# Performance work log

Hardware: AMD Instinct MI355X
Metric: run time of the kernel (lower is better)

The kernel has to match this reference:

```python
import jax, jax.numpy as jnp
import numpy as np
from jax import lax

ALPHABET = 64
E = 1024   # embedding_dim == output_dim == HIDDEN
H = 1024
MSG_LEN = 20
BOS = ALPHABET          # 64
PAD = ALPHABET + 1      # 65
EOS = 0
B = 4096


def setup_inputs() -> dict:
    key = jax.random.key(0)
    ks = jax.random.split(key, 12)
    def u(k, shape, s):
        return jax.random.uniform(k, shape, jnp.float32, -s, s)
    sE = 1.0 / np.sqrt(E)
    sH = 1.0 / np.sqrt(H)
    embed = jax.random.normal(ks[0], (ALPHABET + 2, E), jnp.float32)
    embed = embed.at[PAD].set(0.0)  # padding_idx row is zero
    return dict(
        encoded=jax.random.normal(ks[1], (B, E), jnp.float32),
        embed=embed,
        W_ih=u(ks[2], (4 * H, E), sH), W_hh=u(ks[3], (4 * H, H), sH),
        b_ih=u(ks[4], (4 * H,), sH), b_hh=u(ks[5], (4 * H,), sH),
        W_cell=u(ks[6], (E, E), sE), b_cell=u(ks[7], (E,), sE),
        W_hid=u(ks[8], (E, E), sE), b_hid=u(ks[9], (E,), sE),
        W_act=u(ks[10], (ALPHABET, E), sE), b_act=u(ks[11], (ALPHABET,), sE),
    )


def reference(encoded, embed, W_ih, W_hh, b_ih, b_hh,
              W_cell, b_cell, W_hid, b_hid, W_act, b_act):
    b = encoded.shape[0]
    # torch passes state=(cell, hidden) to nn.LSTM, which reads (h0, c0):
    h0 = encoded @ W_cell.T + b_cell
    c0 = encoded @ W_hid.T + b_hid
    last0 = jnp.full((b,), BOS, jnp.int32)
    stopped0 = jnp.zeros((b,), bool)
    keys = jax.random.split(jax.random.key(42), MSG_LEN)
    bias = b_ih + b_hh

    def step(carry, k):
        h, c, last, stopped = carry
        # embedding lookup; zero the pad row (padding_idx semantics)
        x = embed[last] * (last != PAD)[:, None].astype(embed.dtype)
        gates = x @ W_ih.T + h @ W_hh.T + bias          # [b, 4H], gate order i,f,g,o
        i, f, g, o = jnp.split(gates, 4, axis=-1)
        c2 = jax.nn.sigmoid(f) * c + jax.nn.sigmoid(i) * jnp.tanh(g)
        h2 = jax.nn.sigmoid(o) * jnp.tanh(c2)
        logits = h2 @ W_act.T + b_act                   # [b, ALPHABET]
        action = jax.random.categorical(k, logits)      # training-mode sample
        logp = jax.nn.log_softmax(logits)
        live = (~stopped).astype(logits.dtype)
        ent = -jnp.sum(jnp.exp(logp) * logp, axis=-1) * live
        lp = jnp.take_along_axis(logp, action[:, None], axis=1)[:, 0] * live
        action = jnp.where(stopped, PAD, action).astype(jnp.int32)
        stopped2 = stopped | (action == EOS)
        return (h2, c2, action, stopped2), (action, lp, ent)

    _, (msg, lps, ents) = lax.scan(step, (h0, c0, last0, stopped0), keys)
    msg = msg.T          # [b, MSG_LEN]
    log_probs = lps.T    # [b, MSG_LEN]
    ents = ents.T        # [b, MSG_LEN]
    message_len = jnp.sum(msg != PAD, axis=1, keepdims=True)  # count of non-pad symbols
    entropy = jnp.sum(ents, axis=1, keepdims=True) / message_len.astype(ents.dtype)
    return entropy, log_probs, msg, message_len
```

## Files before the change

### kernel.cpp

```cpp
#include <hip/hip_runtime.h>
#include <stdint.h>

#define ALPHA 64
#define EDIM 1024
#define G4 4096
#define BATCH 4096
#define TLEN 20
#define BOS_TOK 64
#define PAD_TOK 65
#define EOS_TOK 0

__device__ __forceinline__ void threefry2x32(uint32_t k0, uint32_t k1,
                                             uint32_t& x0, uint32_t& x1) {
  uint32_t ks[3] = {k0, k1, k0 ^ k1 ^ 0x1BD11BDAu};
  const int rot0[4] = {13, 15, 26, 6};
  const int rot1[4] = {17, 29, 16, 24};
  x0 += ks[0];
  x1 += ks[1];
#pragma unroll
  for (int i = 0; i < 5; ++i) {
    const int* rr = (i & 1) ? rot1 : rot0;
#pragma unroll
    for (int j = 0; j < 4; ++j) {
      x0 += x1;
      x1 = (x1 << rr[j]) | (x1 >> (32 - rr[j]));
      x1 ^= x0;
    }
    x0 += ks[(i + 1) % 3];
    x1 += ks[(i + 2) % 3] + (uint32_t)(i + 1);
  }
}

__global__ void init_kernel(uint32_t* __restrict__ keyA, uint32_t* __restrict__ keyB,
                            int* __restrict__ last, int* __restrict__ stopped,
                            double* __restrict__ ent_sum, int* __restrict__ len_sum) {
  int i = blockIdx.x * 256 + threadIdx.x;
  if (i < BATCH) {
    last[i] = BOS_TOK;
    stopped[i] = 0;
    ent_sum[i] = 0.0;
    len_sum[i] = 0;
  }
  if (i < TLEN) {
    uint32_t x0 = 0u, x1 = (uint32_t)i;
    threefry2x32(0u, 42u, x0, x1);
    keyA[i] = x0;
    keyB[i] = x1;
  }
}

__global__ void transpose_wact(const float* __restrict__ W, float* __restrict__ Wt) {
  int i = blockIdx.x * 256 + threadIdx.x;
  if (i < ALPHA * EDIM) {
    int a = i >> 10, k = i & 1023;
    Wt[(size_t)k * ALPHA + a] = W[i];
  }
}

template <int MODE>
__global__ __launch_bounds__(256) void gemm_nt(
    const float* __restrict__ A, const float* __restrict__ Bw, float* __restrict__ C,
    int M, int N, int K,
    const float* __restrict__ bias1, const float* __restrict__ bias2,
    const float* __restrict__ eg, const int* __restrict__ lastIdx) {
  __shared__ float As[16][132];
  __shared__ float Bs[16][132];
  const int t = threadIdx.x;
  const int bm = blockIdx.y * 128;
  const int bn = blockIdx.x * 128;
  const int tx = t & 15, ty = t >> 4;

  float acc[8][8];
#pragma unroll
  for (int i = 0; i < 8; ++i)
#pragma unroll
    for (int j = 0; j < 8; ++j) acc[i][j] = 0.0f;

  const int sr = t >> 1;
  const int sc = (t & 1) << 3;
  const float* ap = A + (size_t)(bm + sr) * K + sc;
  const float* bp = Bw + (size_t)(bn + sr) * K + sc;
  const bool aok = (bm + sr) < M;

  for (int k0 = 0; k0 < K; k0 += 16) {
    float4 av0 = {0.f, 0.f, 0.f, 0.f}, av1 = {0.f, 0.f, 0.f, 0.f};
    if (aok) {
      av0 = *(const float4*)(ap + k0);
      av1 = *(const float4*)(ap + k0 + 4);
    }
    float4 bv0 = *(const float4*)(bp + k0);
    float4 bv1 = *(const float4*)(bp + k0 + 4);
    __syncthreads();
    As[sc + 0][sr] = av0.x; As[sc + 1][sr] = av0.y; As[sc + 2][sr] = av0.z; As[sc + 3][sr] = av0.w;
    As[sc + 4][sr] = av1.x; As[sc + 5][sr] = av1.y; As[sc + 6][sr] = av1.z; As[sc + 7][sr] = av1.w;
    Bs[sc + 0][sr] = bv0.x; Bs[sc + 1][sr] = bv0.y; Bs[sc + 2][sr] = bv0.z; Bs[sc + 3][sr] = bv0.w;
    Bs[sc + 4][sr] = bv1.x; Bs[sc + 5][sr] = bv1.y; Bs[sc + 6][sr] = bv1.z; Bs[sc + 7][sr] = bv1.w;
    __syncthreads();
#pragma unroll
    for (int k = 0; k < 16; ++k) {
      float4 a0 = *(const float4*)&As[k][ty * 4];
      float4 a1 = *(const float4*)&As[k][ty * 4 + 64];
      float4 b0 = *(const float4*)&Bs[k][tx * 4];
      float4 b1 = *(const float4*)&Bs[k][tx * 4 + 64];
      float ar[8] = {a0.x, a0.y, a0.z, a0.w, a1.x, a1.y, a1.z, a1.w};
      float br[8] = {b0.x, b0.y, b0.z, b0.w, b1.x, b1.y, b1.z, b1.w};
#pragma unroll
      for (int i = 0; i < 8; ++i)
#pragma unroll
        for (int j = 0; j < 8; ++j) acc[i][j] = fmaf(ar[i], br[j], acc[i][j]);
    }
  }

#pragma unroll
  for (int i = 0; i < 8; ++i) {
    int mG = bm + ty * 4 + (i & 3) + ((i >> 2) << 6);
    if (mG >= M) continue;
    const float* egrow = nullptr;
    if (MODE == 1) egrow = eg + (size_t)lastIdx[mG] * G4;
#pragma unroll
    for (int j = 0; j < 8; ++j) {
      int nG = bn + tx * 4 + (j & 3) + ((j >> 2) << 6);
      float v;
      if (MODE == 0) {
        v = acc[i][j];
        if (bias1) v = __fadd_rn(v, bias1[nG]);
      } else {
        float bsum = __fadd_rn(bias1[nG], bias2[nG]);
        v = __fadd_rn(__fadd_rn(egrow[nG], acc[i][j]), bsum);
      }
      C[(size_t)mG * N + nG] = v;
    }
  }
}

__global__ __launch_bounds__(256) void lstm_pointwise(const float* __restrict__ gates,
                                                      float* __restrict__ h,
                                                      float* __restrict__ c) {
  int idx = blockIdx.x * 256 + threadIdx.x;
  int b = idx >> 10, jj = idx & 1023;
  const float* grow = gates + ((size_t)b << 12);
  float gi = grow[jj];
  float gf = grow[jj + 1024];
  float gg = grow[jj + 2048];
  float go = grow[jj + 3072];
  float cc = c[idx];
  float si = 1.0f / (__fadd_rn(1.0f, expf(-gi)));
  float sf = 1.0f / (__fadd_rn(1.0f, expf(-gf)));
  float so = 1.0f / (__fadd_rn(1.0f, expf(-go)));
  float c2 = __fadd_rn(__fmul_rn(sf, cc), __fmul_rn(si, tanhf(gg)));
  float h2 = __fmul_rn(so, tanhf(c2));
  c[idx] = c2;
  h[idx] = h2;
}

__global__ __launch_bounds__(256) void logits_sample(
    const float* __restrict__ h, const float* __restrict__ Wt,
    const float* __restrict__ b_act,
    const uint32_t* __restrict__ keyA, const uint32_t* __restrict__ keyB, int tstep,
    int* __restrict__ last, int* __restrict__ stopped,
    double* __restrict__ ent_sum, int* __restrict__ len_sum,
    float* __restrict__ out_lp, float* __restrict__ out_msg) {
  __shared__ float Ws[64][64];
  __shared__ float Hs[8][64];
  const int tid = threadIdx.x;
  const int wave = tid >> 6;
  const int lane = tid & 63;
  const int rowBase = blockIdx.x * 8;

  float acc0 = 0.0f, acc1 = 0.0f;
  for (int kp = 0; kp < EDIM; kp += 64) {
    __syncthreads();
    {
      const float4* src = (const float4*)(Wt + (size_t)kp * ALPHA);
      float4* dst = (float4*)&Ws[0][0];
#pragma unroll
      for (int q = 0; q < 4; ++q) dst[tid + q * 256] = src[tid + q * 256];
    }
    if (tid < 128) {
      int rr = tid >> 4;
      int cc = (tid & 15) << 2;
      *(float4*)&Hs[rr][cc] = *(const float4*)(h + (size_t)(rowBase + rr) * EDIM + kp + cc);
    }
    __syncthreads();
#pragma unroll
    for (int kk = 0; kk < 64; ++kk) {
      float w = Ws[kk][lane];
      acc0 = fmaf(Hs[wave * 2 + 0][kk], w, acc0);
      acc1 = fmaf(Hs[wave * 2 + 1][kk], w, acc1);
    }
  }

  const float ba = b_act[lane];
  const uint32_t k0 = keyA[tstep], k1 = keyB[tstep];
  float logitv[2] = {__fadd_rn(acc0, ba), __fadd_rn(acc1, ba)};

#pragma unroll
  for (int rsel = 0; rsel < 2; ++rsel) {
    const int b = rowBase + wave * 2 + rsel;
    const float logit = logitv[rsel];

    uint32_t m = ((uint32_t)b << 6) | (uint32_t)lane;
    uint32_t x0 = 0u, x1 = m;
    threefry2x32(k0, k1, x0, x1);
    uint32_t bits = x0 ^ x1;

    float f = __fsub_rn(__uint_as_float((bits >> 9) | 0x3F800000u), 1.0f);
    const float TINY = 1.17549435e-38f;
    float u = fmaxf(TINY, __fadd_rn(f, TINY));
    float gmb = -logf(-logf(u));
    float z = __fadd_rn(logit, gmb);

    float bv = z;
    int bi = lane;
#pragma unroll
    for (int off = 32; off > 0; off >>= 1) {
      float ov = __shfl_xor(bv, off, 64);
      int oi = __shfl_xor(bi, off, 64);
      if (ov > bv || (ov == bv && oi < bi)) { bv = ov; bi = oi; }
    }

    float mx = logit;
#pragma unroll
    for (int off = 32; off > 0; off >>= 1) mx = fmaxf(mx, __shfl_xor(mx, off, 64));
    float sh = __fsub_rn(logit, mx);
    float e = expf(sh);
    float s = e;
#pragma unroll
    for (int off = 32; off > 0; off >>= 1) s = __fadd_rn(s, __shfl_xor(s, off, 64));
    float ls = logf(s);
    float logp = __fsub_rn(sh, ls);

    float term = __fmul_rn(expf(logp), logp);
    float ts = term;
#pragma unroll
    for (int off = 32; off > 0; off >>= 1) ts = __fadd_rn(ts, __shfl_xor(ts, off, 64));

    float lp_taken = __shfl(logp, bi, 64);

    int st = stopped[b];
    float live = st ? 0.0f : 1.0f;
    int act = st ? PAD_TOK : bi;
    int st2 = (st || act == EOS_TOK) ? 1 : 0;

    if (lane == 0) {
      out_msg[(size_t)b * TLEN + tstep] = (float)act;
      out_lp[(size_t)b * TLEN + tstep] = __fmul_rn(lp_taken, live);
      ent_sum[b] += (double)__fmul_rn(-ts, live);
      len_sum[b] += (act != PAD_TOK) ? 1 : 0;
      last[b] = act;
      stopped[b] = st2;
    }
  }
}

__global__ void finalize_kernel(const double* __restrict__ ent_sum,
                                const int* __restrict__ len_sum,
                                float* __restrict__ out_ent, float* __restrict__ out_len) {
  int b = blockIdx.x * 256 + threadIdx.x;
  if (b < BATCH) {
    out_ent[b] = (float)(ent_sum[b] / (double)len_sum[b]);
    out_len[b] = (float)len_sum[b];
  }
}

extern "C" void kernel_launch(void* const* d_in, const int* in_sizes, int n_in,
                              void* d_out, int out_size, void* d_ws, size_t ws_size,
                              hipStream_t stream) {
  const float* encoded = (const float*)d_in[0];
  const float* embed = (const float*)d_in[1];
  const float* W_ih = (const float*)d_in[2];
  const float* W_hh = (const float*)d_in[3];
  const float* b_ih = (const float*)d_in[4];
  const float* b_hh = (const float*)d_in[5];
  const float* W_cell = (const float*)d_in[6];
  const float* b_cell = (const float*)d_in[7];
  const float* W_hid = (const float*)d_in[8];
  const float* b_hid = (const float*)d_in[9];
  const float* W_act = (const float*)d_in[10];
  const float* b_act = (const float*)d_in[11];

  float* out = (float*)d_out;
  float* out_ent = out;
  float* out_lp = out + BATCH;
  float* out_msg = out + BATCH + BATCH * TLEN;
  float* out_len = out + BATCH + 2 * BATCH * TLEN;

  char* ws = (char*)d_ws;
  size_t off = 0;
  auto alloc = [&](size_t bytes) -> void* {
    void* p = ws + off;
    off = (off + bytes + 255) & ~(size_t)255;
    return p;
  };
  float* h = (float*)alloc(sizeof(float) * (size_t)BATCH * EDIM);
  float* c = (float*)alloc(sizeof(float) * (size_t)BATCH * EDIM);
  float* gates = (float*)alloc(sizeof(float) * (size_t)BATCH * G4);
  float* eg = (float*)alloc(sizeof(float) * 66 * G4);
  float* Wt = (float*)alloc(sizeof(float) * EDIM * ALPHA);
  uint32_t* keyA = (uint32_t*)alloc(sizeof(uint32_t) * TLEN);
  uint32_t* keyB = (uint32_t*)alloc(sizeof(uint32_t) * TLEN);
  int* last = (int*)alloc(sizeof(int) * BATCH);
  int* stopped = (int*)alloc(sizeof(int) * BATCH);
  double* ent_s = (double*)alloc(sizeof(double) * BATCH);
  int* len_s = (int*)alloc(sizeof(int) * BATCH);
  (void)ws_size; (void)in_sizes; (void)n_in; (void)out_size;

  init_kernel<<<16, 256, 0, stream>>>(keyA, keyB, last, stopped, ent_s, len_s);
  transpose_wact<<<(ALPHA * EDIM) / 256, 256, 0, stream>>>(W_act, Wt);

  gemm_nt<0><<<dim3(32, 1), 256, 0, stream>>>(embed, W_ih, eg, 66, G4, EDIM,
                                              nullptr, nullptr, nullptr, nullptr);
  gemm_nt<0><<<dim3(8, 32), 256, 0, stream>>>(encoded, W_cell, h, BATCH, EDIM, EDIM,
                                              b_cell, nullptr, nullptr, nullptr);
  gemm_nt<0><<<dim3(8, 32), 256, 0, stream>>>(encoded, W_hid, c, BATCH, EDIM, EDIM,
                                              b_hid, nullptr, nullptr, nullptr);

  for (int t = 0; t < TLEN; ++t) {
    gemm_nt<1><<<dim3(32, 32), 256, 0, stream>>>(h, W_hh, gates, BATCH, G4, EDIM,
                                                 b_ih, b_hh, eg, last);
    lstm_pointwise<<<(BATCH * EDIM) / 256, 256, 0, stream>>>(gates, h, c);
    logits_sample<<<BATCH / 8, 256, 0, stream>>>(h, Wt, b_act, keyA, keyB, t,
                                                 last, stopped, ent_s, len_s,
                                                 out_lp, out_msg);
  }
  finalize_kernel<<<16, 256, 0, stream>>>(ent_s, len_s, out_ent, out_len);
}
```

Before: 9.178 ms.

## Fuse LSTM pointwise into recurrent GEMM epilogue with gate-interleaved tiles

Each GEMM tile now loads the i/f/g/o rows for 32 hidden units, so every thread holds all four gates for its outputs and applies the LSTM cell update in the epilogue. This removes the 64MB gates buffer write and read-back and one kernel launch per step. Because the fused kernel reads h while writing the new h, h is double-buffered. The epilogue now has strided global accesses to c and h and does transcendental work per thread inside the GEMM kernel.

After: 9.638 ms. +5.0%, slower.

```diff
diff --git a/kernel.cpp b/kernel.cpp
--- a/kernel.cpp
+++ b/kernel.cpp
@@ -57,12 +57,9 @@
   }
 }
 
-template <int MODE>
-__global__ __launch_bounds__(256) void gemm_nt(
+__global__ __launch_bounds__(256) void gemm_nt0(
     const float* __restrict__ A, const float* __restrict__ Bw, float* __restrict__ C,
-    int M, int N, int K,
-    const float* __restrict__ bias1, const float* __restrict__ bias2,
-    const float* __restrict__ eg, const int* __restrict__ lastIdx) {
+    int M, int N, int K, const float* __restrict__ bias1) {
   __shared__ float As[16][132];
   __shared__ float Bs[16][132];
   const int t = threadIdx.x;
@@ -115,42 +112,97 @@
   for (int i = 0; i < 8; ++i) {
     int mG = bm + ty * 4 + (i & 3) + ((i >> 2) << 6);
     if (mG >= M) continue;
-    const float* egrow = nullptr;
-    if (MODE == 1) egrow = eg + (size_t)lastIdx[mG] * G4;
 #pragma unroll
     for (int j = 0; j < 8; ++j) {
       int nG = bn + tx * 4 + (j & 3) + ((j >> 2) << 6);
-      float v;
-      if (MODE == 0) {
-        v = acc[i][j];
-        if (bias1) v = __fadd_rn(v, bias1[nG]);
-      } else {
-        float bsum = __fadd_rn(bias1[nG], bias2[nG]);
-        v = __fadd_rn(__fadd_rn(egrow[nG], acc[i][j]), bsum);
+      float v = acc[i][j];
+      if (bias1) v = __fadd_rn(v, bias1[nG]);
+      C[(size_t)mG * N + nG] = v;
+    }
+  }
+}
+
+__global__ __launch_bounds__(256) void gemm_lstm_fused(
+    const float* __restrict__ A, const float* __restrict__ Bw,
+    const float* __restrict__ eg, const int* __restrict__ lastIdx,
+    const float* __restrict__ b_ih, const float* __restrict__ b_hh,
+    float* __restrict__ hN, float* __restrict__ cst) {
+  __shared__ float As[16][132];
+  __shared__ float Bs[16][132];
+  const int t = threadIdx.x;
+  const int bm = blockIdx.y * 128;
+  const int j0 = blockIdx.x * 32;
+  const int tx = t & 15, ty = t >> 4;
+
+  float acc[8][8];
+#pragma unroll
+  for (int i = 0; i < 8; ++i)
+#pragma unroll
+    for (int j = 0; j < 8; ++j) acc[i][j] = 0.0f;
+
+  const int sr = t >> 1;
+  const int sc = (t & 1) << 3;
+  const float* ap = A + (size_t)(bm + sr) * EDIM + sc;
+  const float* bp = Bw + (size_t)((sr & 3) * EDIM + j0 + (sr >> 2)) * EDIM + sc;
+
+  float4 av0 = *(const float4*)(ap);
+  float4 av1 = *(const float4*)(ap + 4);
+  float4 bv0 = *(const float4*)(bp);
+  float4 bv1 = *(const float4*)(bp + 4);
+
+  for (int k0 = 0; k0 < EDIM; k0 += 16) {
+    __syncthreads();
+    As[sc + 0][sr] = av0.x; As[sc + 1][sr] = av0.y; As[sc + 2][sr] = av0.z; As[sc + 3][sr] = av0.w;
+    As[sc + 4][sr] = av1.x; As[sc + 5][sr] = av1.y; As[sc + 6][sr] = av1.z; As[sc + 7][sr] = av1.w;
+    Bs[sc + 0][sr] = bv0.x; Bs[sc + 1][sr] = bv0.y; Bs[sc + 2][sr] = bv0.z; Bs[sc + 3][sr] = bv0.w;
+    Bs[sc + 4][sr] = bv1.x; Bs[sc + 5][sr] = bv1.y; Bs[sc + 6][sr] = bv1.z; Bs[sc + 7][sr] = bv1.w;
+    if (k0 + 16 < EDIM) {
+      av0 = *(const float4*)(ap + k0 + 16);
+      av1 = *(const float4*)(ap + k0 + 20);
+      bv0 = *(const float4*)(bp + k0 + 16);
+      bv1 = *(const float4*)(bp + k0 + 20);
+    }
+    __syncthreads();
+#pragma unroll
+    for (int k = 0; k < 16; ++k) {
+      float4 a0 = *(const float4*)&As[k][ty * 4];
+      float4 a1 = *(const float4*)&As[k][ty * 4 + 64];
+      float4 b0 = *(const float4*)&Bs[k][tx * 4];
+      float4 b1 = *(const float4*)&Bs[k][tx * 4 + 64];
+      float ar[8] = {a0.x, a0.y, a0.z, a0.w, a1.x, a1.y, a1.z, a1.w};
+      float br[8] = {b0.x, b0.y, b0.z, b0.w, b1.x, b1.y, b1.z, b1.w};
+#pragma unroll
+      for (int i = 0; i < 8; ++i)
+#pragma unroll
+        for (int j = 0; j < 8; ++j) acc[i][j] = fmaf(ar[i], br[j], acc[i][j]);
+    }
+  }
+
+#pragma unroll
+  for (int i = 0; i < 8; ++i) {
+    const int row = bm + ty * 4 + (i & 3) + ((i >> 2) << 6);
+    const float* egrow = eg + (size_t)lastIdx[row] * G4;
+#pragma unroll
+    for (int jj = 0; jj < 2; ++jj) {
+      const int jg = j0 + tx + jj * 16;
+      float gv[4];
+#pragma unroll
+      for (int g = 0; g < 4; ++g) {
+        const int n = g * EDIM + jg;
+        const float bsum = __fadd_rn(b_ih[n], b_hh[n]);
+        gv[g] = __fadd_rn(__fadd_rn(egrow[n], acc[i][jj * 4 + g]), bsum);
       }
-      C[(size_t)mG * N + nG] = v;
-    }
-  }
-}
-
-__global__ __launch_bounds__(256) void lstm_pointwise(const float* __restrict__ gates,
-                                                      float* __restrict__ h,
-                                                      float* __restrict__ c) {
-  int idx = blockIdx.x * 256 + threadIdx.x;
-  int b = idx >> 10, jj = idx & 1023;
-  const float* grow = gates + ((size_t)b << 12);
-  float gi = grow[jj];
-  float gf = grow[jj + 1024];
-  float gg = grow[jj + 2048];
-  float go = grow[jj + 3072];
-  float cc = c[idx];
-  float si = 1.0f / (__fadd_rn(1.0f, expf(-gi)));
-  float sf = 1.0f / (__fadd_rn(1.0f, expf(-gf)));
-  float so = 1.0f / (__fadd_rn(1.0f, expf(-go)));
-  float c2 = __fadd_rn(__fmul_rn(sf, cc), __fmul_rn(si, tanhf(gg)));
-  float h2 = __fmul_rn(so, tanhf(c2));
-  c[idx] = c2;
-  h[idx] = h2;
+      const size_t idx = (size_t)row * EDIM + jg;
+      float cc = cst[idx];
+      float si = 1.0f / (__fadd_rn(1.0f, expf(-gv[0])));
+      float sf = 1.0f / (__fadd_rn(1.0f, expf(-gv[1])));
+      float so = 1.0f / (__fadd_rn(1.0f, expf(-gv[3])));
+      float c2 = __fadd_rn(__fmul_rn(sf, cc), __fmul_rn(si, tanhf(gv[2])));
+      float h2 = __fmul_rn(so, tanhf(c2));
+      cst[idx] = c2;
+      hN[idx] = h2;
+    }
+  }
 }
 
 __global__ __launch_bounds__(256) void logits_sample(
@@ -292,9 +344,9 @@
     off = (off + bytes + 255) & ~(size_t)255;
     return p;
   };
-  float* h = (float*)alloc(sizeof(float) * (size_t)BATCH * EDIM);
+  float* h0b = (float*)alloc(sizeof(float) * (size_t)BATCH * EDIM);
+  float* h1b = (float*)alloc(sizeof(float) * (size_t)BATCH * EDIM);
   float* c = (float*)alloc(sizeof(float) * (size_t)BATCH * EDIM);
-  float* gates = (float*)alloc(sizeof(float) * (size_t)BATCH * G4);
   float* eg = (float*)alloc(sizeof(float) * 66 * G4);
   float* Wt = (float*)alloc(sizeof(float) * EDIM * ALPHA);
   uint32_t* keyA = (uint32_t*)alloc(sizeof(uint32_t) * TLEN);
@@ -308,18 +360,17 @@
   init_kernel<<<16, 256, 0, stream>>>(keyA, keyB, last, stopped, ent_s, len_s);
   transpose_wact<<<(ALPHA * EDIM) / 256, 256, 0, stream>>>(W_act, Wt);
 
-  gemm_nt<0><<<dim3(32, 1), 256, 0, stream>>>(embed, W_ih, eg, 66, G4, EDIM,
-                                              nullptr, nullptr, nullptr, nullptr);
-  gemm_nt<0><<<dim3(8, 32), 256, 0, stream>>>(encoded, W_cell, h, BATCH, EDIM, EDIM,
-                                              b_cell, nullptr, nullptr, nullptr);
-  gemm_nt<0><<<dim3(8, 32), 256, 0, stream>>>(encoded, W_hid, c, BATCH, EDIM, EDIM,
-                                              b_hid, nullptr, nullptr, nullptr);
-
+  gemm_nt0<<<dim3(32, 1), 256, 0, stream>>>(embed, W_ih, eg, 66, G4, EDIM, nullptr);
+  gemm_nt0<<<dim3(8, 32), 256, 0, stream>>>(encoded, W_cell, h0b, BATCH, EDIM, EDIM, b_cell);
+  gemm_nt0<<<dim3(8, 32), 256, 0, stream>>>(encoded, W_hid, c, BATCH, EDIM, EDIM, b_hid);
+
+  float* hb[2] = {h0b, h1b};
   for (int t = 0; t < TLEN; ++t) {
-    gemm_nt<1><<<dim3(32, 32), 256, 0, stream>>>(h, W_hh, gates, BATCH, G4, EDIM,
-                                                 b_ih, b_hh, eg, last);
-    lstm_pointwise<<<(BATCH * EDIM) / 256, 256, 0, stream>>>(gates, h, c);
-    logits_sample<<<BATCH / 8, 256, 0, stream>>>(h, Wt, b_act, keyA, keyB, t,
+    const float* hin = hb[t & 1];
+    float* hout = hb[(t & 1) ^ 1];
+    gemm_lstm_fused<<<dim3(32, 32), 256, 0, stream>>>(hin, W_hh, eg, last,
+                                                      b_ih, b_hh, hout, c);
+    logits_sample<<<BATCH / 8, 256, 0, stream>>>(hout, Wt, b_act, keyA, keyB, t,
                                                  last, stopped, ent_s, len_s,
                                                  out_lp, out_msg);
   }
```
